# Kernel optimization log

Measured on AMD Instinct MI355X. Metric: run time of the kernel, lower is better.

## Reference

```python
import jax, jax.numpy as jnp
import numpy as np

B, S, D, H = 2, 2048, 1024, 16
DK = D // H


def setup_inputs() -> dict:
    key = jax.random.key(0)
    ks = jax.random.split(key, 12)
    scale = 1.0 / np.sqrt(D)
    inp = {
        "q": jax.random.normal(ks[0], (B, S, D), jnp.float32),
        "k": jax.random.normal(ks[1], (B, S, D), jnp.float32),
        "v": jax.random.normal(ks[2], (B, S, D), jnp.float32),
        # causal mask: 1 = attend, 0 = mask, broadcastable to (B, 1, S, S)
        "mask": jnp.tril(jnp.ones((S, S), jnp.int32))[None, None, :, :],
        "Wq": jax.random.normal(ks[3], (D, D), jnp.float32) * scale,
        "bq": jax.random.normal(ks[4], (D,), jnp.float32) * scale,
        "Wk": jax.random.normal(ks[5], (D, D), jnp.float32) * scale,
        "bk": jax.random.normal(ks[6], (D,), jnp.float32) * scale,
        "Wv": jax.random.normal(ks[7], (D, D), jnp.float32) * scale,
        "bv": jax.random.normal(ks[8], (D,), jnp.float32) * scale,
        "Wo": jax.random.normal(ks[9], (D, D), jnp.float32) * scale,
        "bo": jax.random.normal(ks[10], (D,), jnp.float32) * scale,
    }
    return inp


def _split_heads(x):
    b, s, _ = x.shape
    return x.reshape(b, s, H, DK).transpose(0, 2, 1, 3)  # (b, h, s, dk)


def reference(q, k, v, mask, Wq, bq, Wk, bk, Wv, bv, Wo, bo):
    Q = _split_heads(q @ Wq.T + bq)
    K = _split_heads(k @ Wk.T + bk)
    V = _split_heads(v @ Wv.T + bv)
    scores = jnp.einsum("bhqd,bhkd->bhqk", Q, K) * (DK ** -0.5)
    scores = jnp.where(mask == 0, -jnp.inf, scores)
    attn = jax.nn.softmax(scores, axis=-1)  # dropout p=0.0 -> identity
    out = jnp.einsum("bhqk,bhkd->bhqd", attn, V)
    out = out.transpose(0, 2, 1, 3).reshape(q.shape[0], q.shape[1], D)
    return out @ Wo.T + bo
```

## Files before the change

### kernel.cpp

```cpp
#include <hip/hip_runtime.h>


#define S_LEN 2048
#define NHEAD 16
#define DMODEL 1024
#define DKH 64
#define LDT 88

typedef unsigned short u16;
typedef __attribute__((ext_vector_type(4))) short short4v;
typedef __attribute__((ext_vector_type(8))) short short8;
typedef __attribute__((ext_vector_type(8))) __bf16 bf16x8;
typedef __attribute__((ext_vector_type(4))) float f32x4;

__device__ inline u16 f2bf(float f) {
  return __builtin_bit_cast(u16, (__bf16)f);
}

__device__ inline f32x4 mfma16x16(bf16x8 a, bf16x8 b, f32x4 c) {
  return __builtin_amdgcn_mfma_f32_16x16x32_bf16(a, b, c, 0, 0, 0);
}

__device__ inline short8 pack8(float4 a, float4 b) {
  short8 r;
  r[0] = (short)f2bf(a.x); r[1] = (short)f2bf(a.y);
  r[2] = (short)f2bf(a.z); r[3] = (short)f2bf(a.w);
  r[4] = (short)f2bf(b.x); r[5] = (short)f2bf(b.y);
  r[6] = (short)f2bf(b.z); r[7] = (short)f2bf(b.w);
  return r;
}

typedef const __attribute__((address_space(1))) unsigned GU32;
typedef __attribute__((address_space(3))) unsigned LU32;
__device__ inline void gl2lds16(const void* g, void* l) {
  __builtin_amdgcn_global_load_lds((GU32*)g, (LU32*)l, 16, 0, 0);
}

#define SWZ(row, col8) (((row) * 8 + ((col8) ^ ((row) & 7))) * 8)

__global__ __launch_bounds__(256)
void conv_w(const float* __restrict__ w0, const float* __restrict__ w1,
            const float* __restrict__ w2, const float* __restrict__ w3,
            u16* __restrict__ o0, u16* __restrict__ o1,
            u16* __restrict__ o2, u16* __restrict__ o3)
{
  const int z = blockIdx.y;
  const float* s = z == 0 ? w0 : z == 1 ? w1 : z == 2 ? w2 : w3;
  u16* d = z == 0 ? o0 : z == 1 ? o1 : z == 2 ? o2 : o3;
  const int i = (blockIdx.x * 256 + threadIdx.x) * 8;
  float4 a = *(const float4*)&s[i];
  float4 b = *(const float4*)&s[i + 4];
  *(short8*)&d[i] = pack8(a, b);
}

__global__ __launch_bounds__(256)
void proj_gemm(const float* __restrict__ Aq, const float* __restrict__ Akk,
               const float* __restrict__ Av,
               const u16* __restrict__ Bq, const u16* __restrict__ Bk,
               const u16* __restrict__ Bv,
               const float* __restrict__ cq, const float* __restrict__ ck,
               const float* __restrict__ cv,
               u16* __restrict__ Oq, u16* __restrict__ Ok, u16* __restrict__ Ov)
{
  __shared__ u16 SM[2 * 128 * 64];
  u16* As = SM;
  u16* Bs = SM + 128 * 64;

  const int hw = blockIdx.x + (blockIdx.y << 3) + (blockIdx.z << 8);
  const int xcd = hw & 7, sq = hw >> 3;
  const int pan = sq % 12, xb = sq / 12;
  const int p = pan * 8 + xcd;
  const int zz = p >> 5, py = p & 31;

  const float* Af = zz == 0 ? Aq : zz == 1 ? Akk : Av;
  const u16* Wb = zz == 0 ? Bq : zz == 1 ? Bk : Bv;
  const float* bias = zz == 0 ? cq : zz == 1 ? ck : cv;

  const int t = threadIdx.x;
  const int lane = t & 63;
  const int wv = t >> 6;
  const int wm = wv >> 1, wn = wv & 1;
  const int g = lane >> 4, lr = lane & 15;
  const int bm = py << 7, bn = xb << 7;
  const int K = DMODEL;

  f32x4 acc[4][4] = {};
  for (int kt = 0; kt < K / 64; ++kt) {
    const int k0 = kt << 6;
    __syncthreads();
#pragma unroll
    for (int i = 0; i < 4; ++i) {
      int c = t + (i << 8);
      int row = c >> 3, col8 = c & 7;
      int c8s = col8 ^ (row & 7);
      gl2lds16(&Wb[(size_t)(bn + row) * K + k0 + c8s * 8], &Bs[c * 8]);
      const float* src = &Af[(size_t)(bm + row) * K + k0 + col8 * 8];
      float4 x = *(const float4*)src;
      float4 y = *(const float4*)(src + 4);
      *(short8*)&As[SWZ(row, col8)] = pack8(x, y);
    }
    __syncthreads();
    bf16x8 af[2][4], bf[2][4];
#pragma unroll
    for (int kc = 0; kc < 2; ++kc)
#pragma unroll
      for (int f = 0; f < 4; ++f) {
        af[kc][f] = *(const bf16x8*)&As[SWZ(wm * 64 + f * 16 + lr, kc * 4 + g)];
        bf[kc][f] = *(const bf16x8*)&Bs[SWZ(wn * 64 + f * 16 + lr, kc * 4 + g)];
      }
#pragma unroll
    for (int kc = 0; kc < 2; ++kc)
#pragma unroll
      for (int fm = 0; fm < 4; ++fm)
#pragma unroll
        for (int fn = 0; fn < 4; ++fn)
          acc[fm][fn] = mfma16x16(af[kc][fm], bf[kc][fn], acc[fm][fn]);
  }

  if (zz == 2) {
    u16* TL = SM;
    const int b = bm >> 11, s0 = bm & (S_LEN - 1), h0 = bn >> 6;
#pragma unroll
    for (int hh = 0; hh < 2; ++hh) {
      __syncthreads();
      if (wn == hh) {
#pragma unroll
        for (int fm = 0; fm < 4; ++fm)
#pragma unroll
          for (int fn = 0; fn < 4; ++fn) {
            const int lch = fn * 16 + lr;
            const float bb = bias[bn + hh * 64 + lch];
#pragma unroll
            for (int r = 0; r < 4; ++r)
              TL[lch * 132 + wm * 64 + fm * 16 + g * 4 + r] = f2bf(acc[fm][fn][r] + bb);
          }
      }
      __syncthreads();
#pragma unroll
      for (int i = 0; i < 4; ++i) {
        int c = t + (i << 8);
        int dk = c >> 4, sc = (c & 15) << 3;
        short8 vv = *(const short8*)&TL[dk * 132 + sc];
        *(short8*)&Ov[(((size_t)(b * NHEAD + h0 + hh)) * DKH + dk) * S_LEN + s0 + sc] = vv;
      }
    }
  } else {
    u16* Out = zz == 0 ? Oq : Ok;
#pragma unroll
    for (int fm = 0; fm < 4; ++fm)
#pragma unroll
      for (int fn = 0; fn < 4; ++fn) {
        const int col = bn + wn * 64 + fn * 16 + lr;
        const int h = col >> 6, dk = col & (DKH - 1);
        const float bb = bias[col];
#pragma unroll
        for (int r = 0; r < 4; ++r) {
          const int row = bm + wm * 64 + fm * 16 + g * 4 + r;
          const int b = row >> 11, s = row & (S_LEN - 1);
          Out[(((size_t)(b * NHEAD + h)) * S_LEN + s) * DKH + dk] = f2bf(acc[fm][fn][r] + bb);
        }
      }
  }
}

__global__ __launch_bounds__(256)
void out_gemm(const u16* __restrict__ Ao, const u16* __restrict__ Wb,
              const float* __restrict__ bias, float* __restrict__ Out)
{
  __shared__ u16 SM[2 * 128 * 64];
  u16* As = SM;
  u16* Bs = SM + 128 * 64;

  const int hw = blockIdx.x + (blockIdx.y << 3);
  const int xcd = hw & 7, sq = hw >> 3;
  const int pan = sq & 3, xb = sq >> 2;
  const int prow = pan * 8 + xcd;

  const int t = threadIdx.x;
  const int lane = t & 63;
  const int wv = t >> 6;
  const int wm = wv >> 1, wn = wv & 1;
  const int g = lane >> 4, lr = lane & 15;
  const int bm = prow << 7, bn = xb << 7;
  const int K = DMODEL;

  f32x4 acc[4][4] = {};
  for (int kt = 0; kt < K / 64; ++kt) {
    const int k0 = kt << 6;
    __syncthreads();
#pragma unroll
    for (int i = 0; i < 4; ++i) {
      int c = t + (i << 8);
      int row = c >> 3, col8 = c & 7;
      int c8s = col8 ^ (row & 7);
      int grow = bm + row;
      int b = grow >> 11, s = grow & (S_LEN - 1);
      int k = k0 + c8s * 8;
      int h = k >> 6, dk = k & (DKH - 1);
      gl2lds16(&Ao[(((size_t)(b * NHEAD + h)) * S_LEN + s) * DKH + dk], &As[c * 8]);
      gl2lds16(&Wb[(size_t)(bn + row) * K + k0 + c8s * 8], &Bs[c * 8]);
    }
    __syncthreads();
    bf16x8 af[2][4], bf[2][4];
#pragma unroll
    for (int kc = 0; kc < 2; ++kc)
#pragma unroll
      for (int f = 0; f < 4; ++f) {
        af[kc][f] = *(const bf16x8*)&As[SWZ(wm * 64 + f * 16 + lr, kc * 4 + g)];
        bf[kc][f] = *(const bf16x8*)&Bs[SWZ(wn * 64 + f * 16 + lr, kc * 4 + g)];
      }
#pragma unroll
    for (int kc = 0; kc < 2; ++kc)
#pragma unroll
      for (int fm = 0; fm < 4; ++fm)
#pragma unroll
        for (int fn = 0; fn < 4; ++fn)
          acc[fm][fn] = mfma16x16(af[kc][fm], bf[kc][fn], acc[fm][fn]);
  }
#pragma unroll
  for (int fm = 0; fm < 4; ++fm)
#pragma unroll
    for (int fn = 0; fn < 4; ++fn) {
      const int col = bn + wn * 64 + fn * 16 + lr;
      const float bb = bias[col];
#pragma unroll
      for (int r = 0; r < 4; ++r) {
        const int row = bm + wm * 64 + fm * 16 + g * 4 + r;
        Out[(size_t)row * DMODEL + col] = acc[fm][fn][r] + bb;
      }
    }
}

template<bool AF32, int OMODE>
__global__ __launch_bounds__(256)
void gemm64(const void* __restrict__ Ap, const float* __restrict__ Bt,
            const float* __restrict__ bias, void* __restrict__ outp,
            int M, int N, int K)
{
  __shared__ u16 As[64 * LDT];
  __shared__ u16 Bs[64 * LDT];
  const int t = threadIdx.x;
  const int lane = t & 63;
  const int wv = t >> 6;
  const int wm = wv >> 1, wn = wv & 1;
  const int g = lane >> 4, lr = lane & 15;
  const int bm = blockIdx.y << 6, bn = blockIdx.x << 6;

  f32x4 acc[2][2] = {};
  const int nk = K >> 6;
  for (int kt = 0; kt < nk; ++kt) {
    const int k0 = kt << 6;
    __syncthreads();
#pragma unroll
    for (int i = 0; i < 2; ++i) {
      int c = t + (i << 8);
      int row = c >> 3, col = (c & 7) << 3;
      short8 av;
      if (AF32) {
        const float* Af = (const float*)Ap;
        const float4* pa = (const float4*)&Af[(size_t)(bm + row) * K + k0 + col];
        av = pack8(pa[0], pa[1]);
      } else {
        av = *(const short8*)&((const u16*)Ap)[(size_t)(bm + row) * K + k0 + col];
      }
      *(short8*)&As[row * LDT + col] = av;
      const float4* pb = (const float4*)&Bt[(size_t)(bn + row) * K + k0 + col];
      *(short8*)&Bs[row * LDT + col] = pack8(pb[0], pb[1]);
    }
    __syncthreads();
    bf16x8 af[2][2], bfr[2][2];
#pragma unroll
    for (int kc = 0; kc < 2; ++kc) {
#pragma unroll
      for (int fm = 0; fm < 2; ++fm)
        af[kc][fm] = *(const bf16x8*)&As[(wm * 32 + fm * 16 + lr) * LDT + kc * 32 + g * 8];
#pragma unroll
      for (int fn = 0; fn < 2; ++fn)
        bfr[kc][fn] = *(const bf16x8*)&Bs[(wn * 32 + fn * 16 + lr) * LDT + kc * 32 + g * 8];
    }
#pragma unroll
    for (int kc = 0; kc < 2; ++kc)
#pragma unroll
      for (int fm = 0; fm < 2; ++fm)
#pragma unroll
        for (int fn = 0; fn < 2; ++fn)
          acc[fm][fn] = mfma16x16(af[kc][fm], bfr[kc][fn], acc[fm][fn]);
  }
  if (OMODE == 2) {
    u16* TL = As;
    __syncthreads();
#pragma unroll
    for (int fm = 0; fm < 2; ++fm)
#pragma unroll
      for (int fn = 0; fn < 2; ++fn) {
        const int lc = wn * 32 + fn * 16 + lr;
        const float bb = bias[bn + lc];
#pragma unroll
        for (int r = 0; r < 4; ++r) {
          const int lrow = wm * 32 + fm * 16 + g * 4 + r;
          TL[lc * LDT + lrow] = f2bf(acc[fm][fn][r] + bb);
        }
      }
    __syncthreads();
    const int bh = (bm >> 11) * NHEAD + (bn >> 6);
    const int s0 = bm & (S_LEN - 1);
#pragma unroll
    for (int i = 0; i < 2; ++i) {
      int c = t + (i << 8);
      int dr = c >> 3, sc = (c & 7) << 3;
      short8 vv = *(const short8*)&TL[dr * LDT + sc];
      *(short8*)&((u16*)outp)[((size_t)bh * DKH + dr) * S_LEN + s0 + sc] = vv;
    }
  } else {
#pragma unroll
    for (int fm = 0; fm < 2; ++fm)
#pragma unroll
      for (int fn = 0; fn < 2; ++fn) {
        const int col = bn + wn * 32 + fn * 16 + lr;
        const float bb = bias[col];
#pragma unroll
        for (int r = 0; r < 4; ++r) {
          const int row = bm + wm * 32 + fm * 16 + g * 4 + r;
          float vv = acc[fm][fn][r] + bb;
          if (OMODE == 1) {
            int b = row >> 11, s = row & (S_LEN - 1);
            int h = col >> 6, dk = col & (DKH - 1);
            ((u16*)outp)[(((size_t)(b * NHEAD + h)) * S_LEN + s) * DKH + dk] = f2bf(vv);
          } else {
            ((float*)outp)[(size_t)row * N + col] = vv;
          }
        }
      }
  }
}

template<bool HS>
__global__ __launch_bounds__(256)
void attn_fwd(const u16* __restrict__ Qh, const u16* __restrict__ Kh,
              const u16* __restrict__ Vtg, u16* __restrict__ Ao)
{
  __shared__ u16 Ks[2][64 * LDT];
  __shared__ u16 Vs[2][64 * LDT];
  __shared__ u16 Ps[8][16 * LDT];
  const int t = threadIdx.x, lane = t & 63, w = t >> 6;
  const int g = lane >> 4, lr = lane & 15;
  const int bh = blockIdx.y;
  const int pA = blockIdx.x;
  const int tA = pA, tB = 31 - pA;
  const u16* Qb = Qh + (size_t)bh * S_LEN * DKH;
  const u16* Kb = Kh + (size_t)bh * S_LEN * DKH;
  const u16* Vb = Vtg + (size_t)bh * DKH * S_LEN;

  bf16x8 qfA[2], qfB[2];
#pragma unroll
  for (int kc = 0; kc < 2; ++kc) {
    qfA[kc] = *(const bf16x8*)&Qb[(size_t)(tA * 64 + w * 16 + lr) * DKH + kc * 32 + g * 8];
    qfB[kc] = *(const bf16x8*)&Qb[(size_t)(tB * 64 + w * 16 + lr) * DKH + kc * 32 + g * 8];
  }

  f32x4 oA[4] = {}, oB[4] = {};
  float mA = -1e30f, lA = 0.f, mB = -1e30f, lB = 0.f;

  const int r0 = t >> 3;
  const int c0 = (t & 7) << 3;
  short8 kr0, kr1, vr0, vr1;

  auto LOADT = [&](int kt) {
    const int kv0 = kt << 6;
    kr0 = *(const short8*)&Kb[(size_t)(kv0 + r0) * DKH + c0];
    kr1 = *(const short8*)&Kb[(size_t)(kv0 + r0 + 32) * DKH + c0];
    vr0 = *(const short8*)&Vb[(size_t)r0 * S_LEN + kv0 + c0];
    vr1 = *(const short8*)&Vb[(size_t)(r0 + 32) * S_LEN + kv0 + c0];
  };
  auto WRITET = [&](int b) {
    *(short8*)&Ks[b][r0 * LDT + c0] = kr0;
    *(short8*)&Ks[b][(r0 + 32) * LDT + c0] = kr1;
    *(short8*)&Vs[b][r0 * LDT + c0] = vr0;
    *(short8*)&Vs[b][(r0 + 32) * LDT + c0] = vr1;
  };

  auto COMPUTE = [&](int buf, const bf16x8* qf, f32x4* o, float& m, float& l,
                     int pslot, bool diag) {
    f32x4 sf[4];
#pragma unroll
    for (int fk = 0; fk < 4; ++fk) {
      f32x4 a = {};
#pragma unroll
      for (int kc = 0; kc < 2; ++kc) {
        bf16x8 kf = *(const bf16x8*)&Ks[buf][(fk * 16 + lr) * LDT + kc * 32 + g * 8];
        a = mfma16x16(kf, qf[kc], a);
      }
      sf[fk] = a;
    }
    if (diag) {
#pragma unroll
      for (int fk = 0; fk < 4; ++fk)
#pragma unroll
        for (int r = 0; r < 4; ++r)
          if (fk * 16 + 4 * g + r > w * 16 + lr) sf[fk][r] = -1e30f;
    }
    float pm = fmaxf(fmaxf(sf[0][0], sf[0][1]), fmaxf(sf[0][2], sf[0][3]));
#pragma unroll
    for (int fk = 1; fk < 4; ++fk)
      pm = fmaxf(pm, fmaxf(fmaxf(sf[fk][0], sf[fk][1]), fmaxf(sf[fk][2], sf[fk][3])));
    pm = fmaxf(pm, __shfl_xor(pm, 16, 64));
    pm = fmaxf(pm, __shfl_xor(pm, 32, 64));
    float alpha = 1.0f;
    if (!__all(pm - m <= 64.0f)) {
      float mn = fmaxf(m, pm);
      alpha = __expf((m - mn) * 0.125f);
      m = mn;
#pragma unroll
      for (int r = 0; r < 4; ++r) {
        float ar = __shfl(alpha, 4 * g + r, 64);
#pragma unroll
        for (int d = 0; d < 4; ++d) o[d][r] *= ar;
      }
    }
    float rs = 0.f;
#pragma unroll
    for (int fk = 0; fk < 4; ++fk) {
      float p0 = __expf((sf[fk][0] - m) * 0.125f);
      float p1 = __expf((sf[fk][1] - m) * 0.125f);
      float p2 = __expf((sf[fk][2] - m) * 0.125f);
      float p3 = __expf((sf[fk][3] - m) * 0.125f);
      rs += (p0 + p1) + (p2 + p3);
      short4v pk;
      pk[0] = (short)f2bf(p0); pk[1] = (short)f2bf(p1);
      pk[2] = (short)f2bf(p2); pk[3] = (short)f2bf(p3);
      *(short4v*)&Ps[pslot][lr * LDT + fk * 16 + 4 * g] = pk;
    }
    rs += __shfl_xor(rs, 16, 64);
    rs += __shfl_xor(rs, 32, 64);
    l = l * alpha + rs;
#pragma unroll
    for (int kc = 0; kc < 2; ++kc) {
      bf16x8 pf = *(const bf16x8*)&Ps[pslot][lr * LDT + kc * 32 + g * 8];
#pragma unroll
      for (int df = 0; df < 4; ++df) {
        bf16x8 vf = *(const bf16x8*)&Vs[buf][(df * 16 + lr) * LDT + kc * 32 + g * 8];
        o[df] = mfma16x16(pf, vf, o[df]);
      }
    }
  };

  const int nt = tB + 1;
  LOADT(0);
  WRITET(0);
  for (int kt = 0; kt < nt; ++kt) {
    const int cur = kt & 1;
    const bool more = (kt + 1 < nt);
    if (more) LOADT(kt + 1);
    __syncthreads();
    if (kt <= tA) COMPUTE(cur, qfA, oA, mA, lA, w, kt == tA);
    COMPUTE(cur, qfB, oB, mB, lB, 4 + w, kt == tB);
    if (more) WRITET(cur ^ 1);
  }

  float iA[4], iB[4];
#pragma unroll
  for (int r = 0; r < 4; ++r) {
    iA[r] = __builtin_amdgcn_rcpf(__shfl(lA, 4 * g + r, 64));
    iB[r] = __builtin_amdgcn_rcpf(__shfl(lB, 4 * g + r, 64));
  }
  const int b = bh >> 4, h = bh & (NHEAD - 1);
#pragma unroll
  for (int df = 0; df < 4; ++df)
#pragma unroll
    for (int r = 0; r < 4; ++r) {
      const int d = df * 16 + lr;
      const int qa = tA * 64 + w * 16 + g * 4 + r;
      const int qb2 = tB * 64 + w * 16 + g * 4 + r;
      if (HS) {
        Ao[((size_t)bh * S_LEN + qa) * DKH + d] = f2bf(oA[df][r] * iA[r]);
        Ao[((size_t)bh * S_LEN + qb2) * DKH + d] = f2bf(oB[df][r] * iB[r]);
      } else {
        Ao[((size_t)(b * S_LEN + qa)) * DMODEL + h * DKH + d] = f2bf(oA[df][r] * iA[r]);
        Ao[((size_t)(b * S_LEN + qb2)) * DMODEL + h * DKH + d] = f2bf(oB[df][r] * iB[r]);
      }
    }
}

extern "C" void kernel_launch(void* const* d_in, const int* in_sizes, int n_in,
                              void* d_out, int out_size, void* d_ws, size_t ws_size,
                              hipStream_t stream)
{
  (void)in_sizes; (void)n_in; (void)out_size;
  const float* q  = (const float*)d_in[0];
  const float* k  = (const float*)d_in[1];
  const float* v  = (const float*)d_in[2];
  const float* Wq = (const float*)d_in[4];
  const float* bq = (const float*)d_in[5];
  const float* Wk = (const float*)d_in[6];
  const float* bk = (const float*)d_in[7];
  const float* Wv = (const float*)d_in[8];
  const float* bv = (const float*)d_in[9];
  const float* Wo = (const float*)d_in[10];
  const float* bo = (const float*)d_in[11];

  char* ws = (char*)d_ws;
  const size_t MB = 1024 * 1024;

  if (ws_size >= 40 * MB) {
    u16* Wqb = (u16*)(ws);
    u16* Wkb = (u16*)(ws + 2 * MB);
    u16* Wvb = (u16*)(ws + 4 * MB);
    u16* Wob = (u16*)(ws + 6 * MB);
    u16* Qh  = (u16*)(ws + 8 * MB);
    u16* Kh  = (u16*)(ws + 16 * MB);
    u16* Vt  = (u16*)(ws + 24 * MB);
    u16* Ao  = (u16*)(ws + 32 * MB);

    conv_w<<<dim3(512, 4), 256, 0, stream>>>(Wq, Wk, Wv, Wo, Wqb, Wkb, Wvb, Wob);
    proj_gemm<<<dim3(8, 32, 3), 256, 0, stream>>>(q, k, v, Wqb, Wkb, Wvb,
                                                  bq, bk, bv, Qh, Kh, Vt);
    attn_fwd<true><<<dim3(16, 2 * NHEAD), 256, 0, stream>>>(Qh, Kh, Vt, Ao);
    out_gemm<<<dim3(8, 32), 256, 0, stream>>>(Ao, Wob, bo, (float*)d_out);
  } else {
    u16* Qh = (u16*)(ws);
    u16* Kh = (u16*)(ws + 8 * MB);
    u16* Vt = (u16*)(ws + 16 * MB);
    u16* Ao = (u16*)(ws + 24 * MB);
    const int M = 2 * S_LEN, N = DMODEL, K = DMODEL;
    dim3 gg(N / 64, M / 64), bb(256);
    gemm64<true, 1><<<gg, bb, 0, stream>>>(q, Wq, bq, Qh, M, N, K);
    gemm64<true, 1><<<gg, bb, 0, stream>>>(k, Wk, bk, Kh, M, N, K);
    gemm64<true, 2><<<gg, bb, 0, stream>>>(v, Wv, bv, Vt, M, N, K);
    attn_fwd<false><<<dim3(16, 2 * NHEAD), bb, 0, stream>>>(Qh, Kh, Vt, Ao);
    gemm64<false, 0><<<gg, bb, 0, stream>>>(Ao, Wo, bo, d_out, M, N, K);
  }
}
```

Baseline: 139.9 us.

## Double-buffer LDS tiles in projection and output GEMMs to overlap loads

Both the QKV projection GEMM and the output GEMM now prefetch the next K-tile while the MFMA loop runs on the current one. The output GEMM double-buffers both A and B in LDS. The projection GEMM double-buffers the direct-to-LDS B tile and holds the next fp32 A tile in registers, converting and writing it after compute. The aim is to hide global memory latency behind MFMA work, paid for with more LDS per block (48KB and 64KB) and more registers, which may lower occupancy.

```diff
diff --git a/kernel.cpp b/kernel.cpp
--- a/kernel.cpp
+++ b/kernel.cpp
@@ -62,9 +62,10 @@
                const float* __restrict__ cv,
                u16* __restrict__ Oq, u16* __restrict__ Ok, u16* __restrict__ Ov)
 {
-  __shared__ u16 SM[2 * 128 * 64];
+  __shared__ u16 SM[3 * 128 * 64];
   u16* As = SM;
-  u16* Bs = SM + 128 * 64;
+  u16* Bs0 = SM + 8192;
+  u16* Bs1 = SM + 16384;
 
   const int hw = blockIdx.x + (blockIdx.y << 3) + (blockIdx.z << 8);
   const int xcd = hw & 7, sq = hw >> 3;
@@ -84,29 +85,54 @@
   const int bm = py << 7, bn = xb << 7;
   const int K = DMODEL;
 
-  f32x4 acc[4][4] = {};
-  for (int kt = 0; kt < K / 64; ++kt) {
+  float4 ax[4], ay[4];
+  auto ALOAD = [&](int kt) {
     const int k0 = kt << 6;
-    __syncthreads();
+#pragma unroll
+    for (int i = 0; i < 4; ++i) {
+      int c = t + (i << 8);
+      int row = c >> 3, col8 = c & 7;
+      const float* src = &Af[(size_t)(bm + row) * K + k0 + col8 * 8];
+      ax[i] = *(const float4*)src;
+      ay[i] = *(const float4*)(src + 4);
+    }
+  };
+  auto AWRITE = [&]() {
+#pragma unroll
+    for (int i = 0; i < 4; ++i) {
+      int c = t + (i << 8);
+      int row = c >> 3, col8 = c & 7;
+      *(short8*)&As[SWZ(row, col8)] = pack8(ax[i], ay[i]);
+    }
+  };
+  auto BSTAGE = [&](u16* buf, int kt) {
+    const int k0 = kt << 6;
 #pragma unroll
     for (int i = 0; i < 4; ++i) {
       int c = t + (i << 8);
       int row = c >> 3, col8 = c & 7;
       int c8s = col8 ^ (row & 7);
-      gl2lds16(&Wb[(size_t)(bn + row) * K + k0 + c8s * 8], &Bs[c * 8]);
-      const float* src = &Af[(size_t)(bm + row) * K + k0 + col8 * 8];
-      float4 x = *(const float4*)src;
-      float4 y = *(const float4*)(src + 4);
-      *(short8*)&As[SWZ(row, col8)] = pack8(x, y);
-    }
-    __syncthreads();
+      gl2lds16(&Wb[(size_t)(bn + row) * K + k0 + c8s * 8], &buf[c * 8]);
+    }
+  };
+
+  f32x4 acc[4][4] = {};
+  ALOAD(0);
+  BSTAGE(Bs0, 0);
+  AWRITE();
+  __syncthreads();
+  for (int kt = 0; kt < 16; ++kt) {
+    u16* Bcur = (kt & 1) ? Bs1 : Bs0;
+    u16* Bnxt = (kt & 1) ? Bs0 : Bs1;
+    const bool more = (kt + 1 < 16);
+    if (more) { ALOAD(kt + 1); BSTAGE(Bnxt, kt + 1); }
     bf16x8 af[2][4], bf[2][4];
 #pragma unroll
     for (int kc = 0; kc < 2; ++kc)
 #pragma unroll
       for (int f = 0; f < 4; ++f) {
         af[kc][f] = *(const bf16x8*)&As[SWZ(wm * 64 + f * 16 + lr, kc * 4 + g)];
-        bf[kc][f] = *(const bf16x8*)&Bs[SWZ(wn * 64 + f * 16 + lr, kc * 4 + g)];
+        bf[kc][f] = *(const bf16x8*)&Bcur[SWZ(wn * 64 + f * 16 + lr, kc * 4 + g)];
       }
 #pragma unroll
     for (int kc = 0; kc < 2; ++kc)
@@ -115,6 +141,11 @@
 #pragma unroll
         for (int fn = 0; fn < 4; ++fn)
           acc[fm][fn] = mfma16x16(af[kc][fm], bf[kc][fn], acc[fm][fn]);
+    __syncthreads();
+    if (more) {
+      AWRITE();
+      __syncthreads();
+    }
   }
 
   if (zz == 2) {
@@ -167,10 +198,7 @@
 void out_gemm(const u16* __restrict__ Ao, const u16* __restrict__ Wb,
               const float* __restrict__ bias, float* __restrict__ Out)
 {
-  __shared__ u16 SM[2 * 128 * 64];
-  u16* As = SM;
-  u16* Bs = SM + 128 * 64;
-
+  __shared__ u16 SM[4 * 128 * 64];
   const int hw = blockIdx.x + (blockIdx.y << 3);
   const int xcd = hw & 7, sq = hw >> 3;
   const int pan = sq & 3, xb = sq >> 2;
@@ -184,10 +212,10 @@
   const int bm = prow << 7, bn = xb << 7;
   const int K = DMODEL;
 
-  f32x4 acc[4][4] = {};
-  for (int kt = 0; kt < K / 64; ++kt) {
+  auto STAGE = [&](int buf, int kt) {
     const int k0 = kt << 6;
-    __syncthreads();
+    u16* Asb = SM + buf * 8192;
+    u16* Bsb = SM + 16384 + buf * 8192;
 #pragma unroll
     for (int i = 0; i < 4; ++i) {
       int c = t + (i << 8);
@@ -197,17 +225,26 @@
       int b = grow >> 11, s = grow & (S_LEN - 1);
       int k = k0 + c8s * 8;
       int h = k >> 6, dk = k & (DKH - 1);
-      gl2lds16(&Ao[(((size_t)(b * NHEAD + h)) * S_LEN + s) * DKH + dk], &As[c * 8]);
-      gl2lds16(&Wb[(size_t)(bn + row) * K + k0 + c8s * 8], &Bs[c * 8]);
-    }
-    __syncthreads();
+      gl2lds16(&Ao[(((size_t)(b * NHEAD + h)) * S_LEN + s) * DKH + dk], &Asb[c * 8]);
+      gl2lds16(&Wb[(size_t)(bn + row) * K + k0 + c8s * 8], &Bsb[c * 8]);
+    }
+  };
+
+  f32x4 acc[4][4] = {};
+  STAGE(0, 0);
+  __syncthreads();
+  for (int kt = 0; kt < 16; ++kt) {
+    const int cur = kt & 1;
+    if (kt + 1 < 16) STAGE(cur ^ 1, kt + 1);
+    u16* Asb = SM + cur * 8192;
+    u16* Bsb = SM + 16384 + cur * 8192;
     bf16x8 af[2][4], bf[2][4];
 #pragma unroll
     for (int kc = 0; kc < 2; ++kc)
 #pragma unroll
       for (int f = 0; f < 4; ++f) {
-        af[kc][f] = *(const bf16x8*)&As[SWZ(wm * 64 + f * 16 + lr, kc * 4 + g)];
-        bf[kc][f] = *(const bf16x8*)&Bs[SWZ(wn * 64 + f * 16 + lr, kc * 4 + g)];
+        af[kc][f] = *(const bf16x8*)&Asb[SWZ(wm * 64 + f * 16 + lr, kc * 4 + g)];
+        bf[kc][f] = *(const bf16x8*)&Bsb[SWZ(wn * 64 + f * 16 + lr, kc * 4 + g)];
       }
 #pragma unroll
     for (int kc = 0; kc < 2; ++kc)
@@ -216,6 +253,7 @@
 #pragma unroll
         for (int fn = 0; fn < 4; ++fn)
           acc[fm][fn] = mfma16x16(af[kc][fm], bf[kc][fn], acc[fm][fn]);
+    __syncthreads();
   }
 #pragma unroll
   for (int fm = 0; fm < 4; ++fm)
```

Measured after the change: 131.7 us. 5.9% less time.
